# Kernel optimization log

Measured on AMD Instinct MI355X. Metric: run time of the kernel, lower is better.

## Reference

```python
import math
import jax, jax.numpy as jnp
import numpy as np

N, L, C_IMG, D, FF, H, NL, V = 2, 1024, 512, 512, 2048, 8, 4, 8000
EPS_ATTN = 1e-6
EPS_LN = 1e-5


def pos_enc(position, channels):
    # position: (N, L, 1) float. channels assumed even here (256 / 512).
    num = channels // 2
    log_inc = math.log(10000.0) / (num - 1)
    inv = jnp.exp(jnp.arange(num, dtype=position.dtype) * -log_inc)
    st = position * inv.reshape(1, 1, -1)  # (N, L, num)
    return jnp.concatenate([jnp.sin(st), jnp.cos(st)], -1)


def layer_norm(x, s, b):
    m = jnp.mean(x, -1, keepdims=True)
    v = jnp.mean((x - m) ** 2, -1, keepdims=True)
    return (x - m) / jnp.sqrt(v + EPS_LN) * s + b


def causal_linear_attention(x, mask, Wq, bq, Wk, bk, Wv, bv, Wo, bo):
    # x: (N, L, D), mask: (N, L, 1)
    n, l, d = x.shape
    q = (x @ Wq + bq).reshape(n, l, H, -1)
    k = (x @ Wk + bk).reshape(n, l, H, -1)
    v = (x @ Wv + bv).reshape(n, l, H, -1)
    Q = jax.nn.elu(q) + 1.0                       # elu feature map
    K = (jax.nn.elu(k) + 1.0) * mask[:, :, :, None]
    K_cum = jnp.cumsum(K, axis=1)                 # (N, L, H, dk)
    Z = 1.0 / (jnp.einsum('nlhd,nlhd->nlh', Q, K_cum) + EPS_ATTN)
    KV = jnp.cumsum(K[..., :, None] * v[..., None, :], axis=1)  # (N, L, H, dk, dv)
    out = jnp.einsum('nlhd,nlhde->nlhe', Q, KV) * Z[..., None]
    return out.reshape(n, l, d) @ Wo + bo


def encoder_layer(x, mask, p):
    (Wq, bq, Wk, bk, Wv, bv, Wo, bo, W1, b1, W2, b2, s1, be1, s2, be2) = p
    x = x + causal_linear_attention(x, mask, Wq, bq, Wk, bk, Wv, bv, Wo, bo)
    x = layer_norm(x, s1, be1)
    y = jax.nn.gelu(x @ W1 + b1, approximate=False) @ W2 + b2
    return layer_norm(x + y, s2, be2)


def setup_inputs() -> dict:
    key = jax.random.key(0)
    ks = iter(jax.random.split(key, 64))

    def p(shape):
        return jax.random.normal(next(ks), shape, dtype=jnp.float32) * 0.02

    x_img = jax.random.normal(next(ks), (N, L, C_IMG), dtype=jnp.float32)
    x_txt = jax.random.randint(next(ks), (N, L), 0, V)
    pos = jnp.broadcast_to(jnp.arange(L, dtype=jnp.float32)[None, :, None], (N, L, 1))
    pos_r = jnp.floor(pos / 32.0)
    pos_c = jnp.mod(pos, 32.0)
    pos_t = pos
    first_half = (jnp.arange(L) < L // 2).astype(jnp.float32)[None, :, None]
    mask_img = jnp.broadcast_to(first_half, (N, L, 1))
    mask_txt = 1.0 - mask_img

    inp = dict(x_img=x_img, x_txt=x_txt, mask_img=mask_img, mask_txt=mask_txt,
               pos_r=pos_r, pos_c=pos_c, pos_t=pos_t,
               W_ei=p((C_IMG, D)), b_ei=jnp.zeros((D,)),
               emb_txt=p((V, D)),
               Wq=p((NL, D, D)), bq=jnp.zeros((NL, D)),
               Wk=p((NL, D, D)), bk=jnp.zeros((NL, D)),
               Wv=p((NL, D, D)), bv=jnp.zeros((NL, D)),
               Wo=p((NL, D, D)), bo=jnp.zeros((NL, D)),
               W1=p((NL, D, FF)), b1=jnp.zeros((NL, FF)),
               W2=p((NL, FF, D)), b2=jnp.zeros((NL, D)),
               ln1_s=jnp.ones((NL, D)), ln1_b=jnp.zeros((NL, D)),
               ln2_s=jnp.ones((NL, D)), ln2_b=jnp.zeros((NL, D)),
               W_pi=p((D, C_IMG)), b_pi=jnp.zeros((C_IMG,)),
               W_pt=p((D, V)), b_pt=jnp.zeros((V,)))
    return inp


def reference(x_img, x_txt, mask_img, mask_txt, pos_r, pos_c, pos_t,
              W_ei, b_ei, emb_txt,
              Wq, bq, Wk, bk, Wv, bv, Wo, bo, W1, b1, W2, b2,
              ln1_s, ln1_b, ln2_s, ln2_b, W_pi, b_pi, W_pt, b_pt):
    x_mask = mask_img + mask_txt  # (N, L, 1)
    # image embedding
    half = D // 2
    x_pos = jnp.concatenate([pos_enc(pos_r, half), pos_enc(pos_c, D - half)], -1)
    x_emb_img = ((x_img @ W_ei + b_ei) + x_pos) * mask_img
    # text embedding
    x_emb_txt = (emb_txt[x_txt] + pos_enc(pos_t, D)) * mask_txt
    x = x_emb_img + x_emb_txt
    for i in range(NL):
        p = (Wq[i], bq[i], Wk[i], bk[i], Wv[i], bv[i], Wo[i], bo[i],
             W1[i], b1[i], W2[i], b2[i], ln1_s[i], ln1_b[i], ln2_s[i], ln2_b[i])
        x = encoder_layer(x, x_mask, p)
    logit_img = x @ W_pi + b_pi
    logit_txt = x @ W_pt + b_pt
    return (logit_img, logit_txt)
```

## Files before the change

kernel.cpp:

```cpp
#include <hip/hip_runtime.h>
#include <hip/hip_bf16.h>
#include <math.h>

#define NB 2
#define LSEQ 1024
#define DM 512
#define FFD 2048
#define NHEAD 8
#define DKH 64
#define NLAYER 4
#define VOCAB 8000
#define NCHUNK 16
#define NROWS (NB * LSEQ)
#define QS 1536
#define NHEADCAT 8512
#define NHEADPAD 8576

#define OP_NONE 0
#define OP_GELU 2
#define OP_QKV  3
#define OP_PART 4
#define OP_HEAD 5

typedef __attribute__((ext_vector_type(8))) short short8;
typedef __attribute__((ext_vector_type(4))) float f32x4;
typedef __hip_bfloat16 bf16;

__device__ __forceinline__ void cast_tile(
    const float* __restrict__ s, bf16* __restrict__ d, int K, int N,
    int n0, int k0, int tx, int ty)
{
    __shared__ float tile[32][33];
    #pragma unroll
    for (int i = 0; i < 4; ++i) {
        const int k = k0 + ty + 8 * i;
        const int n = n0 + tx;
        tile[ty + 8 * i][tx] = (n < N) ? s[(size_t)k * N + n] : 0.f;
    }
    __syncthreads();
    #pragma unroll
    for (int i = 0; i < 4; ++i) {
        const int n = n0 + ty + 8 * i;
        d[(size_t)n * K + k0 + tx] = __float2bfloat16(tile[tx][ty + 8 * i]);
    }
}

#define CO_QKVO 0
#define CO_W1   4096
#define CO_W2   8192
#define CO_WEI  12288
#define CO_WPI  12544
#define CO_WPT  12800
#define CO_XIMG 16832
#define CO_QKVB 17856
#define CO_HB   17860
#define CO_END  17894

__global__ __launch_bounds__(256) void setup_all(
    const float* __restrict__ Wq, const float* __restrict__ Wk,
    const float* __restrict__ Wv, const float* __restrict__ Wo,
    const float* __restrict__ W1, const float* __restrict__ W2,
    const float* __restrict__ Wei, const float* __restrict__ Wpi,
    const float* __restrict__ Wpt,
    bf16* __restrict__ QKVt, bf16* __restrict__ Wot,
    bf16* __restrict__ W1t, bf16* __restrict__ W2t,
    bf16* __restrict__ Weit, bf16* __restrict__ Whead,
    const float* __restrict__ x_img, bf16* __restrict__ ximgh,
    const float* __restrict__ bq, const float* __restrict__ bk,
    const float* __restrict__ bv, float* __restrict__ qkvB,
    const float* __restrict__ bpi, const float* __restrict__ bpt,
    float* __restrict__ hb)
{
    const int id = blockIdx.x;
    const int tid = threadIdx.x;
    const int tx = tid & 31, ty = tid >> 5;

    if (id < CO_W1) {
        const int rel = id;
        const int z = rel >> 8, t = rel & 255;
        const int layer = z >> 2, which = z & 3;
        const float* src = (which == 0 ? Wq : which == 1 ? Wk : which == 2 ? Wv : Wo)
                           + (size_t)layer * 262144;
        bf16* dst = (which < 3)
            ? (QKVt + (size_t)layer * 786432 + (size_t)which * 262144)
            : (Wot + (size_t)layer * 262144);
        cast_tile(src, dst, 512, 512, (t & 15) * 32, (t >> 4) * 32, tx, ty);
    } else if (id < CO_W2) {
        const int rel = id - CO_W1;
        const int z = rel >> 10, t = rel & 1023;
        cast_tile(W1 + (size_t)z * 1048576, W1t + (size_t)z * 1048576,
                  512, 2048, (t & 63) * 32, (t >> 6) * 32, tx, ty);
    } else if (id < CO_WEI) {
        const int rel = id - CO_W2;
        const int z = rel >> 10, t = rel & 1023;
        cast_tile(W2 + (size_t)z * 1048576, W2t + (size_t)z * 1048576,
                  2048, 512, (t & 15) * 32, (t >> 4) * 32, tx, ty);
    } else if (id < CO_WPI) {
        const int t = id - CO_WEI;
        cast_tile(Wei, Weit, 512, 512, (t & 15) * 32, (t >> 4) * 32, tx, ty);
    } else if (id < CO_WPT) {
        const int t = id - CO_WPI;
        cast_tile(Wpi, Whead, 512, 512, (t & 15) * 32, (t >> 4) * 32, tx, ty);
    } else if (id < CO_XIMG) {
        const int t = id - CO_WPT;
        cast_tile(Wpt, Whead + 262144, 512, VOCAB,
                  (t % 252) * 32, (t / 252) * 32, tx, ty);
    } else if (id < CO_QKVB) {
        const int i = (id - CO_XIMG) * 256 + tid;
        const float4 v = *(const float4*)(x_img + (size_t)i * 4);
        ximgh[(size_t)i * 4 + 0] = __float2bfloat16(v.x);
        ximgh[(size_t)i * 4 + 1] = __float2bfloat16(v.y);
        ximgh[(size_t)i * 4 + 2] = __float2bfloat16(v.z);
        ximgh[(size_t)i * 4 + 3] = __float2bfloat16(v.w);
    } else if (id < CO_HB) {
        const int z = id - CO_QKVB;
        for (int j = tid; j < QS; j += 256) {
            float v;
            if (j < 512)       v = bq[z * DM + j];
            else if (j < 1024) v = bk[z * DM + j - 512];
            else               v = bv[z * DM + j - 1024];
            qkvB[z * QS + j] = v;
        }
    } else {
        const int j = (id - CO_HB) * 256 + tid;
        if (j < NHEADPAD)
            hb[j] = (j < 512) ? bpi[j] : (j < NHEADCAT ? bpt[j - 512] : 0.f);
    }
}

template<int BM, int BN>
__global__ __launch_bounds__(256) void gemm16(
    const bf16* __restrict__ A, const bf16* __restrict__ Bt,
    const float* __restrict__ bias, const float* __restrict__ res,
    float* __restrict__ outF, float* __restrict__ outF2,
    bf16* __restrict__ outH,
    int M, int K, int Nout, int op, int kslab)
{
    constexpr int WM = BM / 2, WN = BN / 2, MI = WM / 16, NI = WN / 16;
    constexpr int LA = BM / 64, LB = BN / 64;
    constexpr int NL = LA + LB;
    __shared__ bf16 As[2][BM * 32];
    __shared__ bf16 Bs[2][BN * 32];
    const int tid = threadIdx.x;
    const int lane = tid & 63;
    const int wave = tid >> 6;
    const int wm = (wave >> 1) * WM, wn = (wave & 1) * WN;

    int bxi = blockIdx.x, byi = blockIdx.y;
    if (op == OP_HEAD) {
        const int gx = gridDim.x;
        const int nwg = gx * gridDim.y;
        int flat = byi * gx + bxi;
        const int q = nwg >> 3, r = nwg & 7;
        const int xcd = flat & 7, lid = flat >> 3;
        flat = (xcd < r ? xcd * (q + 1) : r * (q + 1) + (xcd - r) * q) + lid;
        bxi = flat % gx;
        byi = flat / gx;
    }
    const int bm = (op == OP_HEAD ? bxi : blockIdx.y) * BM;
    const int bn = (op == OP_HEAD ? byi : blockIdx.x) * BN;
    const int l16 = lane & 15, quad = lane >> 4;

    const int rA = tid >> 2;
    const int c8 = (tid & 3) << 3;

    f32x4 acc[MI][NI];
    #pragma unroll
    for (int i = 0; i < MI; ++i)
        #pragma unroll
        for (int j = 0; j < NI; ++j) acc[i][j] = (f32x4){0.f, 0.f, 0.f, 0.f};

    const bf16* gA = A  + (size_t)(bm + rA) * K + c8;
    const bf16* gB = Bt + (size_t)(bn + rA) * K + c8;
    const int ldsWaveOff = wave * 1024;

    const int kStart = blockIdx.z * kslab;
    const int kEnd = kStart + kslab;

    auto stage = [&](int buf, int k0) {
        #pragma unroll
        for (int i = 0; i < LA; ++i)
            __builtin_amdgcn_global_load_lds(
                (const __attribute__((address_space(1))) void*)(gA + (size_t)i * 64 * K + k0),
                (__attribute__((address_space(3))) void*)((char*)As[buf] + i * 4096 + ldsWaveOff),
                16, 0, 0);
        #pragma unroll
        for (int i = 0; i < LB; ++i)
            __builtin_amdgcn_global_load_lds(
                (const __attribute__((address_space(1))) void*)(gB + (size_t)i * 64 * K + k0),
                (__attribute__((address_space(3))) void*)((char*)Bs[buf] + i * 4096 + ldsWaveOff),
                16, 0, 0);
    };

    stage(0, kStart);
    int cur = 0;
    for (int k0 = kStart; k0 < kEnd; k0 += 32) {
        const bool hasNext = (k0 + 32 < kEnd);
        if (hasNext) {
            stage(cur ^ 1, k0 + 32);
            asm volatile("s_waitcnt vmcnt(%0)" :: "n"(NL) : "memory");
        } else {
            asm volatile("s_waitcnt vmcnt(0)" ::: "memory");
        }
        __builtin_amdgcn_s_barrier();
        short8 a[MI], b[NI];
        #pragma unroll
        for (int i = 0; i < MI; ++i)
            a[i] = *(const short8*)(As[cur] + (size_t)(wm + i * 16 + l16) * 32 + quad * 8);
        #pragma unroll
        for (int j = 0; j < NI; ++j)
            b[j] = *(const short8*)(Bs[cur] + (size_t)(wn + j * 16 + l16) * 32 + quad * 8);
        #pragma unroll
        for (int i = 0; i < MI; ++i)
            #pragma unroll
            for (int j = 0; j < NI; ++j)
                acc[i][j] = __builtin_amdgcn_mfma_f32_16x16x32_bf16(
                    a[i], b[j], acc[i][j], 0, 0, 0);
        __builtin_amdgcn_s_barrier();
        cur ^= 1;
    }

    if (op == OP_PART) {
        float* dst = outF + (size_t)blockIdx.z * (size_t)M * Nout;
        #pragma unroll
        for (int j = 0; j < NI; ++j) {
            const int col = bn + wn + j * 16 + l16;
            #pragma unroll
            for (int i = 0; i < MI; ++i)
                #pragma unroll
                for (int r = 0; r < 4; ++r) {
                    const int row = bm + wm + i * 16 + quad * 4 + r;
                    dst[(size_t)row * Nout + col] = acc[i][j][r];
                }
        }
        return;
    }
    if (op == OP_HEAD) {
        #pragma unroll
        for (int j = 0; j < NI; ++j) {
            const int col = bn + wn + j * 16 + l16;
            const bool cok = (col < NHEADCAT);
            const float bz = cok ? bias[col] : 0.f;
            #pragma unroll
            for (int i = 0; i < MI; ++i)
                #pragma unroll
                for (int r = 0; r < 4; ++r) {
                    const int row = bm + wm + i * 16 + quad * 4 + r;
                    const float v = acc[i][j][r] + bz;
                    if (cok) {
                        if (col < 512) outF[(size_t)row * 512 + col] = v;
                        else           outF2[(size_t)row * VOCAB + (col - 512)] = v;
                    }
                }
        }
        return;
    }

    #pragma unroll
    for (int j = 0; j < NI; ++j) {
        const int col = bn + wn + j * 16 + l16;
        const bool cok = (col < Nout);
        const float bz = cok ? bias[col] : 0.f;
        #pragma unroll
        for (int i = 0; i < MI; ++i) {
            #pragma unroll
            for (int r = 0; r < 4; ++r) {
                const int row = bm + wm + i * 16 + quad * 4 + r;
                float v = acc[i][j][r] + bz;
                if (op == OP_GELU)      v = 0.5f * v * (1.f + erff(v * 0.70710678118654752f));
                else if (op == OP_QKV && col < 1024) v = (v > 0.f) ? v + 1.f : expf(v);
                if (cok) {
                    if (res)  v += res[(size_t)row * Nout + col];
                    if (outF) outF[(size_t)row * Nout + col] = v;
                    if (outH) outH[(size_t)row * Nout + col] = __float2bfloat16(v);
                }
            }
        }
    }
}

__global__ __launch_bounds__(256) void embed_k(
    const float* __restrict__ gI, const int* __restrict__ xt,
    const float* __restrict__ emb,
    const float* __restrict__ mi, const float* __restrict__ mt,
    const float* __restrict__ pr, const float* __restrict__ pc,
    const float* __restrict__ pt, float* __restrict__ X, bf16* __restrict__ Xh)
{
    const int row = blockIdx.x;
    const float prv = pr[row], pcv = pc[row], ptv = pt[row];
    const float miv = mi[row], mtv = mt[row];
    const int tok = xt[row];
    const float LOG1E4 = 9.2103403719761836f;
    const float LI127 = LOG1E4 / 127.f;
    const float LI255 = LOG1E4 / 255.f;

    for (int d = threadIdx.x; d < DM; d += 256) {
        float ip;
        if (d < 128)       ip = sinf(prv * expf(-(float)d * LI127));
        else if (d < 256)  ip = cosf(prv * expf(-(float)(d - 128) * LI127));
        else if (d < 384)  ip = sinf(pcv * expf(-(float)(d - 256) * LI127));
        else               ip = cosf(pcv * expf(-(float)(d - 384) * LI127));
        float tp;
        if (d < 256) tp = sinf(ptv * expf(-(float)d * LI255));
        else         tp = cosf(ptv * expf(-(float)(d - 256) * LI255));
        const float v = miv * (gI[(size_t)row * DM + d] + ip)
                      + mtv * (emb[(size_t)tok * DM + d] + tp);
        X[(size_t)row * DM + d] = v;
        Xh[(size_t)row * DM + d] = __float2bfloat16(v);
    }
}

__global__ __launch_bounds__(256) void ln_red(
    const float* __restrict__ P, int nP,
    const float* __restrict__ bias, const float* __restrict__ res,
    const float* __restrict__ g, const float* __restrict__ b,
    float* __restrict__ out, bf16* __restrict__ outh)
{
    const int row = blockIdx.x;
    const int tid = threadIdx.x;
    const int lane = tid & 63, wv = tid >> 6;
    const size_t base = (size_t)row * DM;
    float x0 = res[base + tid] + bias[tid];
    float x1 = res[base + tid + 256] + bias[tid + 256];
    for (int p = 0; p < nP; ++p) {
        x0 += P[(size_t)p * 1048576 + base + tid];
        x1 += P[(size_t)p * 1048576 + base + tid + 256];
    }
    __shared__ float redA[4];
    __shared__ float redB[4];
    float s = x0 + x1;
    #pragma unroll
    for (int off = 32; off > 0; off >>= 1) s += __shfl_down(s, off);
    if (lane == 0) redA[wv] = s;
    __syncthreads();
    const float mean = (redA[0] + redA[1] + redA[2] + redA[3]) * (1.f / (float)DM);
    const float d0 = x0 - mean, d1 = x1 - mean;
    float v = d0 * d0 + d1 * d1;
    #pragma unroll
    for (int off = 32; off > 0; off >>= 1) v += __shfl_down(v, off);
    if (lane == 0) redB[wv] = v;
    __syncthreads();
    const float var = (redB[0] + redB[1] + redB[2] + redB[3]) * (1.f / (float)DM);
    const float rstd = rsqrtf(var + 1e-5f);
    const float y0 = d0 * rstd * g[tid] + b[tid];
    const float y1 = d1 * rstd * g[tid + 256] + b[tid + 256];
    out[base + tid]        = y0;
    out[base + tid + 256]  = y1;
    outh[base + tid]       = __float2bfloat16(y0);
    outh[base + tid + 256] = __float2bfloat16(y1);
}

__global__ __launch_bounds__(256) void attn_kv(
    const float* __restrict__ Kp, const float* __restrict__ Vp,
    float* __restrict__ S, float* __restrict__ ks)
{
    const int c = blockIdx.x, h = blockIdx.y, n = blockIdx.z;
    const int tid = threadIdx.x;
    __shared__ float sK[64][64], sV[64][64], part[4][64];

    const int lr = tid >> 4;
    const int c4 = (tid & 15) * 4;
    #pragma unroll
    for (int it = 0; it < 4; ++it) {
        const int row = it * 16 + lr;
        const size_t gb = ((size_t)(n * LSEQ + c * 64 + row)) * QS + h * DKH + c4;
        *(float4*)&sK[row][c4] = *(const float4*)(Kp + gb);
        *(float4*)&sV[row][c4] = *(const float4*)(Vp + gb);
    }
    __syncthreads();

    const int e = tid & 63, dq = tid >> 6;
    float s[16] = {};
    for (int l = 0; l < 64; ++l) {
        const float vv = sV[l][e];
        const float4 k0 = *(const float4*)&sK[l][dq * 16 + 0];
        const float4 k1 = *(const float4*)&sK[l][dq * 16 + 4];
        const float4 k2 = *(const float4*)&sK[l][dq * 16 + 8];
        const float4 k3 = *(const float4*)&sK[l][dq * 16 + 12];
        s[0]  = fmaf(k0.x, vv, s[0]);  s[1]  = fmaf(k0.y, vv, s[1]);
        s[2]  = fmaf(k0.z, vv, s[2]);  s[3]  = fmaf(k0.w, vv, s[3]);
        s[4]  = fmaf(k1.x, vv, s[4]);  s[5]  = fmaf(k1.y, vv, s[5]);
        s[6]  = fmaf(k1.z, vv, s[6]);  s[7]  = fmaf(k1.w, vv, s[7]);
        s[8]  = fmaf(k2.x, vv, s[8]);  s[9]  = fmaf(k2.y, vv, s[9]);
        s[10] = fmaf(k2.z, vv, s[10]); s[11] = fmaf(k2.w, vv, s[11]);
        s[12] = fmaf(k3.x, vv, s[12]); s[13] = fmaf(k3.y, vv, s[13]);
        s[14] = fmaf(k3.z, vv, s[14]); s[15] = fmaf(k3.w, vv, s[15]);
    }
    const size_t sb = (((size_t)(n * NHEAD + h)) * NCHUNK + c) * 4096;
    #pragma unroll
    for (int i = 0; i < 16; ++i) S[sb + (size_t)(dq * 16 + i) * 64 + e] = s[i];

    float kp = 0.f;
    #pragma unroll
    for (int i = 0; i < 16; ++i) kp += sK[dq * 16 + i][e];
    part[dq][e] = kp;
    __syncthreads();
    if (tid < 64)
        ks[(((size_t)(n * NHEAD + h)) * NCHUNK + c) * 64 + tid] =
            part[0][tid] + part[1][tid] + part[2][tid] + part[3][tid];
}

__global__ __launch_bounds__(256) void attn_out(
    const float* __restrict__ QKV, const float* __restrict__ S,
    const float* __restrict__ ks, bf16* __restrict__ O)
{
    const int c = blockIdx.x, h = blockIdx.y, n = blockIdx.z;
    const int tid = threadIdx.x;
    __shared__ float sQt[64][64];
    __shared__ float sKt[64][64];
    __shared__ float sV [64][64];
    __shared__ float sS [64][64];
    __shared__ float sPt[64][65];
    __shared__ float skp[64];

    const size_t nhS = ((size_t)(n * NHEAD + h)) * NCHUNK * 4096;
    const size_t nhK = ((size_t)(n * NHEAD + h)) * NCHUNK * 64;

    {
        float4 aS[4] = {};
        for (int cc = 0; cc < c; ++cc) {
            const float* Sc = S + nhS + (size_t)cc * 4096;
            #pragma unroll
            for (int i = 0; i < 4; ++i) {
                const float4 t = *(const float4*)(Sc + i * 1024 + tid * 4);
                aS[i].x += t.x; aS[i].y += t.y; aS[i].z += t.z; aS[i].w += t.w;
            }
        }
        float* sSf = &sS[0][0];
        #pragma unroll
        for (int i = 0; i < 4; ++i)
            *(float4*)(sSf + i * 1024 + tid * 4) = aS[i];
        if (tid < 64) {
            float kp = 0.f;
            for (int cc = 0; cc < c; ++cc) kp += ks[nhK + cc * 64 + tid];
            skp[tid] = kp;
        }
    }

    const int lr = tid >> 4;
    const int c4 = (tid & 15) * 4;
    #pragma unroll
    for (int it = 0; it < 4; ++it) {
        const int row = it * 16 + lr;
        const size_t gb = ((size_t)(n * LSEQ + c * 64 + row)) * QS + h * DKH + c4;
        const float4 q4 = *(const float4*)(QKV + gb);
        const float4 k4 = *(const float4*)(QKV + gb + 512);
        const float4 v4 = *(const float4*)(QKV + gb + 1024);
        sQt[c4 + 0][row] = q4.x; sQt[c4 + 1][row] = q4.y;
        sQt[c4 + 2][row] = q4.z; sQt[c4 + 3][row] = q4.w;
        sKt[c4 + 0][row] = k4.x; sKt[c4 + 1][row] = k4.y;
        sKt[c4 + 2][row] = k4.z; sKt[c4 + 3][row] = k4.w;
        *(float4*)&sV[row][c4] = v4;
    }
    __syncthreads();

    const int m4 = (tid & 15) * 4;
    const int lg = tid >> 4;
    {
        float p[4][4] = {};
        for (int d = 0; d < 64; ++d) {
            const float4 k4 = *(const float4*)&sKt[d][m4];
            const float4 q4 = *(const float4*)&sQt[d][lg * 4];
            p[0][0] = fmaf(q4.x, k4.x, p[0][0]); p[0][1] = fmaf(q4.x, k4.y, p[0][1]);
            p[0][2] = fmaf(q4.x, k4.z, p[0][2]); p[0][3] = fmaf(q4.x, k4.w, p[0][3]);
            p[1][0] = fmaf(q4.y, k4.x, p[1][0]); p[1][1] = fmaf(q4.y, k4.y, p[1][1]);
            p[1][2] = fmaf(q4.y, k4.z, p[1][2]); p[1][3] = fmaf(q4.y, k4.w, p[1][3]);
            p[2][0] = fmaf(q4.z, k4.x, p[2][0]); p[2][1] = fmaf(q4.z, k4.y, p[2][1]);
            p[2][2] = fmaf(q4.z, k4.z, p[2][2]); p[2][3] = fmaf(q4.z, k4.w, p[2][3]);
            p[3][0] = fmaf(q4.w, k4.x, p[3][0]); p[3][1] = fmaf(q4.w, k4.y, p[3][1]);
            p[3][2] = fmaf(q4.w, k4.z, p[3][2]); p[3][3] = fmaf(q4.w, k4.w, p[3][3]);
        }
        #pragma unroll
        for (int jj = 0; jj < 4; ++jj)
            #pragma unroll
            for (int j = 0; j < 4; ++j)
                sPt[m4 + jj][lg * 4 + j] = p[j][jj];
    }
    __syncthreads();

    float acc[4][4] = {};
    float z[4] = {};
    const int lmax = lg * 4 + 3;
    for (int m = 0; m <= lmax; ++m) {
        const float4 v4 = *(const float4*)&sV[m][m4];
        #pragma unroll
        for (int j = 0; j < 4; ++j) {
            const int l = lg * 4 + j;
            float p = sPt[m][l];
            p = (m <= l) ? p : 0.f;
            z[j] += p;
            acc[j][0] = fmaf(p, v4.x, acc[j][0]);
            acc[j][1] = fmaf(p, v4.y, acc[j][1]);
            acc[j][2] = fmaf(p, v4.z, acc[j][2]);
            acc[j][3] = fmaf(p, v4.w, acc[j][3]);
        }
    }
    for (int d = 0; d < 64; ++d) {
        const float4 s4 = *(const float4*)&sS[d][m4];
        const float4 q4 = *(const float4*)&sQt[d][lg * 4];
        const float kp = skp[d];
        z[0] = fmaf(q4.x, kp, z[0]); z[1] = fmaf(q4.y, kp, z[1]);
        z[2] = fmaf(q4.z, kp, z[2]); z[3] = fmaf(q4.w, kp, z[3]);
        acc[0][0] = fmaf(q4.x, s4.x, acc[0][0]); acc[0][1] = fmaf(q4.x, s4.y, acc[0][1]);
        acc[0][2] = fmaf(q4.x, s4.z, acc[0][2]); acc[0][3] = fmaf(q4.x, s4.w, acc[0][3]);
        acc[1][0] = fmaf(q4.y, s4.x, acc[1][0]); acc[1][1] = fmaf(q4.y, s4.y, acc[1][1]);
        acc[1][2] = fmaf(q4.y, s4.z, acc[1][2]); acc[1][3] = fmaf(q4.y, s4.w, acc[1][3]);
        acc[2][0] = fmaf(q4.z, s4.x, acc[2][0]); acc[2][1] = fmaf(q4.z, s4.y, acc[2][1]);
        acc[2][2] = fmaf(q4.z, s4.z, acc[2][2]); acc[2][3] = fmaf(q4.z, s4.w, acc[2][3]);
        acc[3][0] = fmaf(q4.w, s4.x, acc[3][0]); acc[3][1] = fmaf(q4.w, s4.y, acc[3][1]);
        acc[3][2] = fmaf(q4.w, s4.z, acc[3][2]); acc[3][3] = fmaf(q4.w, s4.w, acc[3][3]);
    }
    #pragma unroll
    for (int j = 0; j < 4; ++j) {
        const int l = lg * 4 + j;
        const float rz = 1.f / (z[j] + 1e-6f);
        const size_t ob = ((size_t)(n * LSEQ + c * 64 + l)) * DM + h * DKH + m4;
        O[ob + 0] = __float2bfloat16(acc[j][0] * rz);
        O[ob + 1] = __float2bfloat16(acc[j][1] * rz);
        O[ob + 2] = __float2bfloat16(acc[j][2] * rz);
        O[ob + 3] = __float2bfloat16(acc[j][3] * rz);
    }
}

extern "C" void kernel_launch(void* const* d_in, const int* in_sizes, int n_in,
                              void* d_out, int out_size, void* d_ws, size_t ws_size,
                              hipStream_t stream)
{
    const float* x_img   = (const float*)d_in[0];
    const int*   x_txt   = (const int*)  d_in[1];
    const float* mask_i  = (const float*)d_in[2];
    const float* mask_t  = (const float*)d_in[3];
    const float* pos_r   = (const float*)d_in[4];
    const float* pos_c   = (const float*)d_in[5];
    const float* pos_t   = (const float*)d_in[6];
    const float* W_ei    = (const float*)d_in[7];
    const float* b_ei    = (const float*)d_in[8];
    const float* emb_txt = (const float*)d_in[9];
    const float* Wq      = (const float*)d_in[10];
    const float* bq      = (const float*)d_in[11];
    const float* Wk      = (const float*)d_in[12];
    const float* bk      = (const float*)d_in[13];
    const float* Wv      = (const float*)d_in[14];
    const float* bv      = (const float*)d_in[15];
    const float* Wo      = (const float*)d_in[16];
    const float* bo      = (const float*)d_in[17];
    const float* W1      = (const float*)d_in[18];
    const float* b1      = (const float*)d_in[19];
    const float* W2      = (const float*)d_in[20];
    const float* b2      = (const float*)d_in[21];
    const float* ln1_s   = (const float*)d_in[22];
    const float* ln1_b   = (const float*)d_in[23];
    const float* ln2_s   = (const float*)d_in[24];
    const float* ln2_b   = (const float*)d_in[25];
    const float* W_pi    = (const float*)d_in[26];
    const float* b_pi    = (const float*)d_in[27];
    const float* W_pt    = (const float*)d_in[28];
    const float* b_pt    = (const float*)d_in[29];

    float* ws = (float*)d_ws;
    size_t off = 0;
    auto alloc = [&](size_t nfloats) { float* p = ws + off; off += nfloats; return p; };

    float* Xb   = alloc(1048576);
    float* Pb   = alloc(4194304);
    float* QKVb = alloc(3145728);
    float* Sb   = alloc(1048576);
    float* ksb  = alloc(16384);
    float* qkvB = alloc(4 * QS);
    float* hb   = alloc(8704);
    bf16* Xh    = (bf16*)alloc(524288);
    bf16* Ob    = (bf16*)alloc(524288);
    bf16* Tb    = (bf16*)alloc(2097152);
    bf16* ximgh = (bf16*)alloc(524288);
    bf16* QKVt  = (bf16*)alloc(1572864);
    bf16* Wot   = (bf16*)alloc(524288);
    bf16* W1t   = (bf16*)alloc(2097152);
    bf16* W2t   = (bf16*)alloc(2097152);
    bf16* Weit  = (bf16*)alloc(131072);
    bf16* Whead = (bf16*)alloc(2195456);

    const dim3 blk(256);
    const dim3 gAttn(NCHUNK, NHEAD, NB);

    setup_all<<<dim3(CO_END), blk, 0, stream>>>(
        Wq, Wk, Wv, Wo, W1, W2, W_ei, W_pi, W_pt,
        QKVt, Wot, W1t, W2t, Weit, Whead,
        x_img, ximgh, bq, bk, bv, qkvB, b_pi, b_pt, hb);

    gemm16<64, 64><<<dim3(8, 32), blk, 0, stream>>>(
        ximgh, Weit, b_ei, nullptr, Pb, nullptr, nullptr, NROWS, 512, 512, OP_NONE, 512);
    embed_k<<<NROWS, blk, 0, stream>>>(Pb, x_txt, emb_txt, mask_i, mask_t,
                                       pos_r, pos_c, pos_t, Xb, Xh);

    for (int i = 0; i < NLAYER; ++i) {
        gemm16<64, 128><<<dim3(12, 32), blk, 0, stream>>>(
            Xh, QKVt + (size_t)i * 786432, qkvB + i * QS, nullptr,
            QKVb, nullptr, nullptr, NROWS, 512, QS, OP_QKV, 512);

        attn_kv<<<gAttn, blk, 0, stream>>>(QKVb + 512, QKVb + 1024, Sb, ksb);
        attn_out<<<gAttn, blk, 0, stream>>>(QKVb, Sb, ksb, Ob);

        gemm16<64, 64><<<dim3(8, 32, 2), blk, 0, stream>>>(
            Ob, Wot + (size_t)i * 262144, nullptr, nullptr,
            Pb, nullptr, nullptr, NROWS, 512, 512, OP_PART, 256);
        ln_red<<<NROWS, blk, 0, stream>>>(Pb, 2, bo + (size_t)i * DM, Xb,
                                          ln1_s + (size_t)i * DM,
                                          ln1_b + (size_t)i * DM, Xb, Xh);

        gemm16<64, 128><<<dim3(16, 32), blk, 0, stream>>>(
            Xh, W1t + (size_t)i * 1048576, b1 + (size_t)i * FFD, nullptr,
            nullptr, nullptr, Tb, NROWS, 512, FFD, OP_GELU, 512);
        gemm16<64, 64><<<dim3(8, 32, 4), blk, 0, stream>>>(
            Tb, W2t + (size_t)i * 1048576, nullptr, nullptr,
            Pb, nullptr, nullptr, NROWS, 2048, 512, OP_PART, 512);
        ln_red<<<NROWS, blk, 0, stream>>>(Pb, 4, b2 + (size_t)i * DM, Xb,
                                          ln2_s + (size_t)i * DM,
                                          ln2_b + (size_t)i * DM, Xb, Xh);
    }

    float* out = (float*)d_out;
    gemm16<128, 128><<<dim3(16, 67), blk, 0, stream>>>(
        Xh, Whead, hb, nullptr, out, out + 1048576, nullptr,
        NROWS, 512, NHEADCAT, OP_HEAD, 512);
}
```

Baseline: 631.0 us.

## Triple-buffer GEMM LDS staging and vectorize weight cast transpose

The GEMM main loop moves from double to triple buffering, issuing global-to-LDS loads two K-steps ahead so more memory latency is hidden behind MFMA work. This raises LDS use per block by half, which may reduce occupancy. Separately, the setup cast kernel now reads float4 and writes 4 bf16 values per thread as 8-byte stores, replacing scalar accesses, and adds a trailing barrier so the shared tile can be reused safely.

```diff
diff --git a/kernel.cpp b/kernel.cpp
--- a/kernel.cpp
+++ b/kernel.cpp
@@ -28,21 +28,28 @@
 
 __device__ __forceinline__ void cast_tile(
     const float* __restrict__ s, bf16* __restrict__ d, int K, int N,
-    int n0, int k0, int tx, int ty)
+    int n0, int k0, int tid)
 {
     __shared__ float tile[32][33];
-    #pragma unroll
-    for (int i = 0; i < 4; ++i) {
-        const int k = k0 + ty + 8 * i;
-        const int n = n0 + tx;
-        tile[ty + 8 * i][tx] = (n < N) ? s[(size_t)k * N + n] : 0.f;
-    }
-    __syncthreads();
-    #pragma unroll
-    for (int i = 0; i < 4; ++i) {
-        const int n = n0 + ty + 8 * i;
-        d[(size_t)n * K + k0 + tx] = __float2bfloat16(tile[tx][ty + 8 * i]);
-    }
+    const int r  = tid >> 3;
+    const int c4 = (tid & 7) * 4;
+    const int n  = n0 + c4;
+    float4 v = make_float4(0.f, 0.f, 0.f, 0.f);
+    if (n < N)
+        v = *(const float4*)(s + (size_t)(k0 + r) * N + n);
+    tile[r][c4 + 0] = v.x; tile[r][c4 + 1] = v.y;
+    tile[r][c4 + 2] = v.z; tile[r][c4 + 3] = v.w;
+    __syncthreads();
+    const int nr = tid >> 3;
+    const int kc = (tid & 7) * 4;
+    bf16 o[4];
+    o[0] = __float2bfloat16(tile[kc + 0][nr]);
+    o[1] = __float2bfloat16(tile[kc + 1][nr]);
+    o[2] = __float2bfloat16(tile[kc + 2][nr]);
+    o[3] = __float2bfloat16(tile[kc + 3][nr]);
+    *(unsigned long long*)(d + (size_t)(n0 + nr) * K + k0 + kc) =
+        *(const unsigned long long*)o;
+    __syncthreads();
 }
 
 #define CO_QKVO 0
@@ -73,7 +80,6 @@
 {
     const int id = blockIdx.x;
     const int tid = threadIdx.x;
-    const int tx = tid & 31, ty = tid >> 5;
 
     if (id < CO_W1) {
         const int rel = id;
@@ -84,27 +90,27 @@
         bf16* dst = (which < 3)
             ? (QKVt + (size_t)layer * 786432 + (size_t)which * 262144)
             : (Wot + (size_t)layer * 262144);
-        cast_tile(src, dst, 512, 512, (t & 15) * 32, (t >> 4) * 32, tx, ty);
+        cast_tile(src, dst, 512, 512, (t & 15) * 32, (t >> 4) * 32, tid);
     } else if (id < CO_W2) {
         const int rel = id - CO_W1;
         const int z = rel >> 10, t = rel & 1023;
         cast_tile(W1 + (size_t)z * 1048576, W1t + (size_t)z * 1048576,
-                  512, 2048, (t & 63) * 32, (t >> 6) * 32, tx, ty);
+                  512, 2048, (t & 63) * 32, (t >> 6) * 32, tid);
     } else if (id < CO_WEI) {
         const int rel = id - CO_W2;
         const int z = rel >> 10, t = rel & 1023;
         cast_tile(W2 + (size_t)z * 1048576, W2t + (size_t)z * 1048576,
-                  2048, 512, (t & 15) * 32, (t >> 4) * 32, tx, ty);
+                  2048, 512, (t & 15) * 32, (t >> 4) * 32, tid);
     } else if (id < CO_WPI) {
         const int t = id - CO_WEI;
-        cast_tile(Wei, Weit, 512, 512, (t & 15) * 32, (t >> 4) * 32, tx, ty);
+        cast_tile(Wei, Weit, 512, 512, (t & 15) * 32, (t >> 4) * 32, tid);
     } else if (id < CO_WPT) {
         const int t = id - CO_WPI;
-        cast_tile(Wpi, Whead, 512, 512, (t & 15) * 32, (t >> 4) * 32, tx, ty);
+        cast_tile(Wpi, Whead, 512, 512, (t & 15) * 32, (t >> 4) * 32, tid);
     } else if (id < CO_XIMG) {
         const int t = id - CO_WPT;
         cast_tile(Wpt, Whead + 262144, 512, VOCAB,
-                  (t % 252) * 32, (t / 252) * 32, tx, ty);
+                  (t % 252) * 32, (t / 252) * 32, tid);
     } else if (id < CO_QKVB) {
         const int i = (id - CO_XIMG) * 256 + tid;
         const float4 v = *(const float4*)(x_img + (size_t)i * 4);
@@ -139,8 +145,8 @@
     constexpr int WM = BM / 2, WN = BN / 2, MI = WM / 16, NI = WN / 16;
     constexpr int LA = BM / 64, LB = BN / 64;
     constexpr int NL = LA + LB;
-    __shared__ bf16 As[2][BM * 32];
-    __shared__ bf16 Bs[2][BN * 32];
+    __shared__ bf16 As[3][BM * 32];
+    __shared__ bf16 Bs[3][BN * 32];
     const int tid = threadIdx.x;
     const int lane = tid & 63;
     const int wave = tid >> 6;
@@ -193,11 +199,15 @@
     };
 
     stage(0, kStart);
+    if (kStart + 32 < kEnd) stage(1, kStart + 32);
     int cur = 0;
     for (int k0 = kStart; k0 < kEnd; k0 += 32) {
-        const bool hasNext = (k0 + 32 < kEnd);
-        if (hasNext) {
-            stage(cur ^ 1, k0 + 32);
+        const int k2 = k0 + 64;
+        if (k2 < kEnd) {
+            int nb = cur + 2; if (nb >= 3) nb -= 3;
+            stage(nb, k2);
+            asm volatile("s_waitcnt vmcnt(%0)" :: "n"(2 * NL) : "memory");
+        } else if (k0 + 32 < kEnd) {
             asm volatile("s_waitcnt vmcnt(%0)" :: "n"(NL) : "memory");
         } else {
             asm volatile("s_waitcnt vmcnt(0)" ::: "memory");
@@ -217,7 +227,7 @@
                 acc[i][j] = __builtin_amdgcn_mfma_f32_16x16x32_bf16(
                     a[i], b[j], acc[i][j], 0, 0, 0);
         __builtin_amdgcn_s_barrier();
-        cur ^= 1;
+        ++cur; if (cur >= 3) cur -= 3;
     }
 
     if (op == OP_PART) {
```

Result: no change. 631.1 us (+0.0%).
